# Optimization experiments

Hardware: AMD Instinct MI355X
Metric: run time of the kernel (lower is better)

The kernel has to match this reference:

```python
import jax, jax.numpy as jnp
import numpy as np

D, T, HID, Q = 33, 49, 64, 64


def _lin(x, w, b):
    return x @ w.T + b


def setup_inputs() -> dict:
    key = jax.random.key(0)
    ks = jax.random.split(key, 40)

    def nrm(k, shape, scale=0.1):
        return jax.random.normal(k, shape, jnp.float32) * scale

    vals = nrm(ks[0], (D, T), 1.0)
    mask = (jax.random.uniform(ks[1], (D, T)) < 0.8).astype(jnp.float32)
    delta = jax.random.uniform(ks[2], (D, T)) * 2.0
    data = jnp.stack([vals, mask, delta])  # [3, 33, 49]

    return {
        "data": data,
        "h0": nrm(ks[3], (HID,), 1.0),
        "H0": nrm(ks[4], (D, HID), 1.0),
        "gh_w": nrm(ks[5], (HID, D)), "gh_b": nrm(ks[6], (HID,)),
        "gst_w": nrm(ks[7], (HID, D)), "gst_b": nrm(ks[8], (HID,)),
        "gru_wih": nrm(ks[9], (3 * HID, D)), "gru_whh": nrm(ks[10], (3 * HID, HID)),
        "gru_bih": nrm(ks[11], (3 * HID,)), "gru_bhh": nrm(ks[12], (3 * HID,)),
        "wu0_w": nrm(ks[13], (Q, HID)), "wu0_b": nrm(ks[14], (Q,)),
        "wu1_w": nrm(ks[15], (Q, 2 * HID)), "wu1_b": nrm(ks[16], (Q,)),
        "wu_w": nrm(ks[17], (Q, 3 * HID)), "wu_b": nrm(ks[18], (Q,)),
        "wh_w": nrm(ks[19], (D, HID + Q)), "wh_b": nrm(ks[20], (D,)),
        "xst_w": nrm(ks[21], (1, HID)), "xst_b": nrm(ks[22], (1,)),
        "wrg_w": nrm(ks[23], (D, HID)),
        "wrs": nrm(ks[24], (1, HID)),
        "tWz": nrm(ks[25], (D, HID, HID)), "tUzx": nrm(ks[26], (D, HID, 1)), "tUzh": nrm(ks[27], (D, HID, HID)),
        "tWr": nrm(ks[28], (D, HID, HID)), "tUrx": nrm(ks[29], (D, HID, 1)), "tUrh": nrm(ks[30], (D, HID, HID)),
        "tWh": nrm(ks[31], (D, HID, HID)), "tUhx": nrm(ks[32], (D, HID, 1)), "tUhh": nrm(ks[33], (D, HID, HID)),
        "tbz": nrm(ks[34], (HID, 1)), "tbr": nrm(ks[35], (HID, 1)), "tbh": nrm(ks[36], (HID, 1)),
    }


def reference(data, h0, H0, gh_w, gh_b, gst_w, gst_b, gru_wih, gru_whh,
              gru_bih, gru_bhh, wu0_w, wu0_b, wu1_w, wu1_b, wu_w, wu_b,
              wh_w, wh_b, xst_w, xst_b, wrg_w, wrs, tWz, tUzx, tUzh,
              tWr, tUrx, tUrh, tWh, tUhx, tUhh, tbz, tbr, tbh):
    X, M, Dt = data[0], data[1], data[2]  # each (33, 49)
    h = h0          # (HID,) -> becomes (1, HID) after first GRUCell step
    H = H0          # (D, HID)
    outs, Hs, xps = [], [], []
    for t in range(T):
        x, m, d = X[:, t], M[:, t], Dt[:, t]
        # GRU-D style decay gate: exp(-max(0, Linear(delta)))
        gamma_h = jnp.exp(-jax.nn.relu(_lin(d, gh_w, gh_b)))
        h = gamma_h * h
        x_st = _lin(H, xst_w, xst_b).reshape(-1)       # (D,)
        x_st_c = m * x + (1 - m) * x_st                # imputed input
        # torch nn.GRUCell
        xi = x_st_c.reshape(1, D)
        hi = h.reshape(1, HID)
        gi = _lin(xi, gru_wih, gru_bih)
        gh_ = _lin(hi, gru_whh, gru_bhh)
        i_r, i_z, i_n = jnp.split(gi, 3, axis=1)
        h_r, h_z, h_n = jnp.split(gh_, 3, axis=1)
        r = jax.nn.sigmoid(i_r + h_r)
        z = jax.nn.sigmoid(i_z + h_z)
        n = jnp.tanh(i_n + r * h_n)
        h = (1 - z) * n + z * hi                       # (1, HID)
        # original detaches the history used for u_t
        outs.append(jax.lax.stop_gradient(h))
        if t == 0:
            u_t = _lin(h0.reshape(1, -1), wu0_w, wu0_b)
        elif t == 1:
            hd = jnp.concatenate([h0.reshape(1, -1), outs[0]], 0).reshape(1, -1)
            u_t = _lin(hd, wu1_w, wu1_b)
        elif t == 2:
            hd = jnp.concatenate([h0.reshape(1, -1), outs[0], outs[1]], 0).reshape(1, -1)
            u_t = _lin(hd, wu_w, wu_b)
        else:
            hd = jnp.concatenate(outs[t - 3:t], 0).reshape(1, -1)
            u_t = _lin(hd, wu_w, wu_b)
        x_gt_hat = _lin(jnp.concatenate([h, u_t], axis=1), wh_w, wh_b)  # (1, D)
        gamma_st = jnp.exp(-jax.nn.relu(_lin(d, gst_w, gst_b)))
        H = gamma_st * H
        # tMGRU cell: per-variable (D=33) batched matmuls
        Hr = H[:, :, None]              # (D, HID, 1)
        xr = x_st_c[:, None, None]      # (D, 1, 1)
        hr = h.reshape(HID, 1)          # (HID, 1)
        z_t = jax.nn.sigmoid(tWz @ Hr + tUzx @ xr + tUzh @ hr + tbz)
        r_t = jax.nn.sigmoid(tWr @ Hr + tUrx @ xr + tUrh @ hr + tbr)
        Hh = jnp.tanh(r_t * (tWh @ Hr) + tUhx @ xr + tUhh @ hr + tbh)
        H = (z_t * Hr + (1 - z_t) * Hh).reshape(D, HID)
        Hs.append(H)
        a = h @ wrg_w.T                 # (1, D)
        b = wrs @ H.T                   # (1, D)
        alpha1 = jax.nn.softmax(a / (a + b), axis=-1)
        alpha2 = jax.nn.softmax(b / (a + b), axis=-1)
        xps.append(alpha1 * x_gt_hat + alpha2 * x_st)  # (1, D)
    H_s = jnp.stack(Hs)                         # (T, D, HID)
    x_pred = jnp.concatenate(xps, axis=0).T     # (D, T)
    return H_s, x_pred
```

## Files before the change

### kernel.cpp

```cpp
#include <hip/hip_runtime.h>
#include <math.h>

#define DD 33
#define TT 49
#define HH 64
#define NB 33
#define NT 256

#define O_WIHT  0
#define O_WHHT  6336
#define O_GH    18624
#define O_GS    21760
#define O_WT0   24896
#define O_WT1   27008
#define O_WTG   31232
#define O_CU    37568
#define O_R     37700
#define O_PF    40936
#define PF_STRIDE 160
#define PREP_N  37700

#define SC_AGENT __HIP_MEMORY_SCOPE_AGENT

__device__ __forceinline__ float sigm(float x) {
  return 1.f / (1.f + __expf(-x));
}
__device__ __forceinline__ float ftanh(float x) {
  x = fminf(fmaxf(x, -15.f), 15.f);
  float e = __expf(2.f * x);
  return (e - 1.f) / (e + 1.f);
}

__device__ __forceinline__ float rsum64(float v) {
#pragma unroll
  for (int o = 32; o > 0; o >>= 1) v += __shfl_xor(v, o, 64);
  return v;
}
__device__ __forceinline__ float rmax64(float v) {
#pragma unroll
  for (int o = 32; o > 0; o >>= 1) v = fmaxf(v, __shfl_xor(v, o, 64));
  return v;
}

extern "C" __global__ void gmgru_prep(
    const float* __restrict__ data, const float* __restrict__ gh_w,
    const float* __restrict__ gh_b, const float* __restrict__ gst_w,
    const float* __restrict__ gst_b, const float* __restrict__ wih,
    const float* __restrict__ whh, const float* __restrict__ wu0,
    const float* __restrict__ wu0b, const float* __restrict__ wu1,
    const float* __restrict__ wu1b, const float* __restrict__ wu,
    const float* __restrict__ wub, const float* __restrict__ wh_w,
    float* __restrict__ ws) {
  int idx = blockIdx.x * blockDim.x + threadIdx.x;
  if (idx < 6336) {
    int k = idx / 192, j = idx % 192;
    ws[O_WIHT + idx] = wih[j * DD + k];
  } else if (idx < 18624) {
    int r = idx - 6336, k = r / 192, j = r % 192;
    ws[O_WHHT + r] = whh[j * HH + k];
  } else if (idx < 21760) {
    int r = idx - 18624, t = r / 64, i = r % 64;
    float s = gh_b[i];
    for (int d2 = 0; d2 < DD; ++d2)
      s += data[2 * DD * TT + d2 * TT + t] * gh_w[i * DD + d2];
    ws[O_GH + r] = expf(-fmaxf(s, 0.f));
  } else if (idx < 24896) {
    int r = idx - 21760, t = r / 64, i = r % 64;
    float s = gst_b[i];
    for (int d2 = 0; d2 < DD; ++d2)
      s += data[2 * DD * TT + d2 * TT + t] * gst_w[i * DD + d2];
    ws[O_GS + r] = expf(-fmaxf(s, 0.f));
  } else if (idx < 27008) {
    int r = idx - 24896, dd = r / 64, k = r % 64;
    float s = 0.f;
    for (int q = 0; q < 64; ++q) s += wu0[q * 64 + k] * wh_w[dd * 128 + 64 + q];
    ws[O_WT0 + r] = s;
  } else if (idx < 31232) {
    int r = idx - 27008, dd = r / 128, k = r % 128;
    float s = 0.f;
    for (int q = 0; q < 64; ++q) s += wu1[q * 128 + k] * wh_w[dd * 128 + 64 + q];
    ws[O_WT1 + r] = s;
  } else if (idx < 37568) {
    int r = idx - 31232, dd = r / 192, k = r % 192;
    float s = 0.f;
    for (int q = 0; q < 64; ++q) s += wu[q * 192 + k] * wh_w[dd * 128 + 64 + q];
    ws[O_WTG + r] = s;
  } else if (idx < PREP_N) {
    int r = idx - 37568, dd = r / 4, v = r % 4;
    float s = 0.f;
    if (v < 3) {
      const float* bp = (v == 0) ? wu0b : (v == 1) ? wu1b : wub;
      for (int q = 0; q < 64; ++q) s += bp[q] * wh_w[dd * 128 + 64 + q];
    }
    ws[O_CU + r] = s;
  }
}

extern "C" __global__ void __launch_bounds__(NT, 1)
gmgru_main(const float* __restrict__ data, const float* __restrict__ h0,
           const float* __restrict__ H0, const float* __restrict__ bih,
           const float* __restrict__ bhh, const float* __restrict__ wh_w,
           const float* __restrict__ wh_b, const float* __restrict__ xst_w,
           const float* __restrict__ xst_b, const float* __restrict__ wrg_w,
           const float* __restrict__ wrs, const float* __restrict__ tWz,
           const float* __restrict__ tUzx, const float* __restrict__ tUzh,
           const float* __restrict__ tWr, const float* __restrict__ tUrx,
           const float* __restrict__ tUrh, const float* __restrict__ tWh,
           const float* __restrict__ tUhx, const float* __restrict__ tUhh,
           const float* __restrict__ tbz, const float* __restrict__ tbr,
           const float* __restrict__ tbh, float* __restrict__ ws,
           unsigned long long* __restrict__ pf, float* __restrict__ out) {
  __shared__ float whhT_l[12288];
  __shared__ float wihT_l[6336];
  __shared__ float part[2][6][4][HH];
  __shared__ float ghL[3 * HH], giL[3 * HH];
  __shared__ float xrow[TT], mrow[TT];

  const int tid = threadIdx.x;
  const int dd = blockIdx.x;
  const int wid = tid >> 6;
  const int lane = tid & 63;

  for (int i = tid; i < 12288; i += NT) whhT_l[i] = ws[O_WHHT + i];
  for (int i = tid; i < 6336; i += NT) wihT_l[i] = ws[O_WIHT + i];
  if (tid < TT) {
    xrow[tid] = data[dd * TT + tid];
    mrow[tid] = data[DD * TT + dd * TT + tid];
  }
  float4 u0[4], u1[4], u2[4];
  {
    const int base = dd * 4096 + lane * 64 + wid * 16;
#pragma unroll
    for (int g = 0; g < 4; ++g) {
      u0[g] = *reinterpret_cast<const float4*>(tUzh + base + g * 4);
      u1[g] = *reinterpret_cast<const float4*>(tUrh + base + g * 4);
      u2[g] = *reinterpret_cast<const float4*>(tUhh + base + g * 4);
    }
  }
  const float bih_r = (tid < 192) ? bih[tid] : 0.f;
  const float bhh_r = (tid < 192) ? bhh[tid] : 0.f;
  const float ux0 = tUzx[dd * HH + lane];
  const float ux1 = tUrx[dd * HH + lane];
  const float ux2 = tUhx[dd * HH + lane];
  const float tb0 = tbz[lane];
  const float tb1 = tbr[lane];
  const float tb2 = tbh[lane];
  const float xstw_r = xst_w[lane];
  const float wrg_r = wrg_w[dd * HH + lane];
  const float wrs_r = wrs[lane];
  const float whr0_r = wh_w[dd * 128 + lane];
  const float wtg0_r = ws[O_WTG + dd * 192 + lane];
  const float wtg1_r = ws[O_WTG + dd * 192 + 64 + lane];
  const float wtg2_r = ws[O_WTG + dd * 192 + 128 + lane];
  const float wt0_r = ws[O_WT0 + dd * 64 + lane];
  const float wt1a_r = ws[O_WT1 + dd * 128 + lane];
  const float wt1b_r = ws[O_WT1 + dd * 128 + 64 + lane];
  const float cu0_r = ws[O_CU + dd * 4 + 0];
  const float cu1_r = ws[O_CU + dd * 4 + 1];
  const float cu2_r = ws[O_CU + dd * 4 + 2];
  const float whb_r = wh_b[dd];
  const float xstb_r = xst_b[0];
  const float h0s_r = h0[lane];
  float hprev = h0s_r;
  float Hrow = H0[dd * HH + lane];
  float gH_cur = ws[O_GH + lane];
  float gS_cur = ws[O_GS + lane];
  __syncthreads();

  float xst_cur = rsum64(Hrow * xstw_r) + xstb_r;
  if (wid == 0 && lane == 0) {
    float xc0 = mrow[0] * xrow[0] + (1.f - mrow[0]) * xst_cur;
    unsigned long long pk0 =
        (1ULL << 32) | (unsigned long long)__float_as_uint(xc0);
    __hip_atomic_store(&pf[(size_t)dd * PF_STRIDE], pk0, __ATOMIC_RELAXED,
                       SC_AGENT);
  }
  float xg_m1 = 0.f, xg_m2 = 0.f, xs_m1 = 0.f, xs_m2 = 0.f;
  float h1 = 0.f, h2 = 0.f, h3 = 0.f;

  for (int t = 0; t < TT; ++t) {
    const int b = t & 1;
    float hpre_r = gH_cur * hprev;
    float Hdec_r = gS_cur * Hrow;
    float gH_nxt = 0.f, gS_nxt = 0.f;
    if (t + 1 < TT) {
      gH_nxt = ws[O_GH + (t + 1) * HH + lane];
      gS_nxt = ws[O_GS + (t + 1) * HH + lane];
    }

    {
      float pw0 = 0.f, pw1 = 0.f, pw2 = 0.f;
      const int base = dd * 4096 + lane * 64 + wid * 16;
#pragma unroll
      for (int g = 0; g < 4; ++g) {
        float4 a = *reinterpret_cast<const float4*>(tWz + base + g * 4);
        float4 bb = *reinterpret_cast<const float4*>(tWr + base + g * 4);
        float4 c = *reinterpret_cast<const float4*>(tWh + base + g * 4);
        float v0 = __shfl(Hdec_r, wid * 16 + g * 4 + 0, 64);
        float v1 = __shfl(Hdec_r, wid * 16 + g * 4 + 1, 64);
        float v2 = __shfl(Hdec_r, wid * 16 + g * 4 + 2, 64);
        float v3 = __shfl(Hdec_r, wid * 16 + g * 4 + 3, 64);
        pw0 += a.x * v0 + a.y * v1 + a.z * v2 + a.w * v3;
        pw1 += bb.x * v0 + bb.y * v1 + bb.z * v2 + bb.w * v3;
        pw2 += c.x * v0 + c.y * v1 + c.z * v2 + c.w * v3;
      }
      part[b][0][wid][lane] = pw0;
      part[b][1][wid][lane] = pw1;
      part[b][2][wid][lane] = pw2;
    }
    if (tid < 3 * HH) {
      float a0 = 0.f, a1 = 0.f, a2 = 0.f, a3 = 0.f;
#pragma unroll
      for (int k = 0; k < HH; k += 4) {
        a0 += whhT_l[(k + 0) * 192 + tid] * __shfl(hpre_r, k + 0, 64);
        a1 += whhT_l[(k + 1) * 192 + tid] * __shfl(hpre_r, k + 1, 64);
        a2 += whhT_l[(k + 2) * 192 + tid] * __shfl(hpre_r, k + 2, 64);
        a3 += whhT_l[(k + 3) * 192 + tid] * __shfl(hpre_r, k + 3, 64);
      }
      ghL[tid] = bhh_r + ((a0 + a1) + (a2 + a3));
    }
    __syncthreads();

    const unsigned tagv = (unsigned)(t + 1);
    unsigned long long pk;
    for (;;) {
      pk = (lane < NB)
               ? __hip_atomic_load(&pf[(size_t)lane * PF_STRIDE + t],
                                   __ATOMIC_RELAXED, SC_AGENT)
               : (((unsigned long long)tagv) << 32);
      if (__all((int)((unsigned)(pk >> 32) == tagv))) break;
      __builtin_amdgcn_s_sleep(1);
    }
    float xcv = __uint_as_float((unsigned)(pk & 0xFFFFFFFFull));
    asm volatile("" ::: "memory");

    if (tid < 3 * HH) {
      float gi = bih_r;
#pragma unroll
      for (int k = 0; k < DD; ++k)
        gi += wihT_l[k * 192 + tid] * __shfl(xcv, k, 64);
      giL[tid] = gi;
    }
    __syncthreads();

    float rg = sigm(giL[lane] + ghL[lane]);
    float zg = sigm(giL[64 + lane] + ghL[64 + lane]);
    float ng = ftanh(giL[128 + lane] + rg * ghL[128 + lane]);
    float hn = (1.f - zg) * ng + zg * hpre_r;

    {
      float pu0 = 0.f, pu1 = 0.f, pu2 = 0.f;
#pragma unroll
      for (int g = 0; g < 4; ++g) {
        float v0 = __shfl(hn, wid * 16 + g * 4 + 0, 64);
        float v1 = __shfl(hn, wid * 16 + g * 4 + 1, 64);
        float v2 = __shfl(hn, wid * 16 + g * 4 + 2, 64);
        float v3 = __shfl(hn, wid * 16 + g * 4 + 3, 64);
        pu0 += u0[g].x * v0 + u0[g].y * v1 + u0[g].z * v2 + u0[g].w * v3;
        pu1 += u1[g].x * v0 + u1[g].y * v1 + u1[g].z * v2 + u1[g].w * v3;
        pu2 += u2[g].x * v0 + u2[g].y * v1 + u2[g].z * v2 + u2[g].w * v3;
      }
      part[b][3][wid][lane] = pu0;
      part[b][4][wid][lane] = pu1;
      part[b][5][wid][lane] = pu2;
    }
    __syncthreads();

    float r1v = -INFINITY, r2v = -INFINITY;
    if (wid == 1 && t >= 2 && lane < DD) {
      r1v = __hip_atomic_load(&ws[O_R + (t - 2) * 66 + lane], __ATOMIC_RELAXED,
                              SC_AGENT);
      r2v = __hip_atomic_load(&ws[O_R + (t - 2) * 66 + 33 + lane],
                              __ATOMIC_RELAXED, SC_AGENT);
    }

    float sz = part[b][0][0][lane] + part[b][0][1][lane] + part[b][0][2][lane] +
               part[b][0][3][lane] + part[b][3][0][lane] + part[b][3][1][lane] +
               part[b][3][2][lane] + part[b][3][3][lane];
    float sr = part[b][1][0][lane] + part[b][1][1][lane] + part[b][1][2][lane] +
               part[b][1][3][lane] + part[b][4][0][lane] + part[b][4][1][lane] +
               part[b][4][2][lane] + part[b][4][3][lane];
    float swh = part[b][2][0][lane] + part[b][2][1][lane] +
                part[b][2][2][lane] + part[b][2][3][lane];
    float suh = part[b][5][0][lane] + part[b][5][1][lane] +
                part[b][5][2][lane] + part[b][5][3][lane];
    float xc = __shfl(xcv, dd, 64);
    float z2 = sigm(sz + ux0 * xc + tb0);
    float r2g = sigm(sr + ux1 * xc + tb1);
    float hh = ftanh(r2g * swh + ux2 * xc + suh + tb2);
    float Hn = z2 * Hdec_r + (1.f - z2) * hh;

    if (wid == 0) {
      float xsn = rsum64(xstw_r * Hn);
      if (lane == 0 && t < TT - 1) {
        float xstv = xsn + xstb_r;
        float xcn = mrow[t + 1] * xrow[t + 1] + (1.f - mrow[t + 1]) * xstv;
        unsigned long long pkn =
            (((unsigned long long)(unsigned)(t + 2)) << 32) |
            (unsigned long long)__float_as_uint(xcn);
        __hip_atomic_store(&pf[(size_t)dd * PF_STRIDE + (t + 1)], pkn,
                           __ATOMIC_RELAXED, SC_AGENT);
      }
    } else if (wid == 1) {
      if (t >= 2) {
        float m1 = rmax64(r1v), m2 = rmax64(r2v);
        float e1 = (lane < DD) ? __expf(r1v - m1) : 0.f;
        float e2 = (lane < DD) ? __expf(r2v - m2) : 0.f;
        float s1 = rsum64(e1), s2 = rsum64(e2);
        float r1o = __shfl(r1v, dd, 64);
        float r2o = __shfl(r2v, dd, 64);
        if (lane == 0) {
          float a1 = __expf(r1o - m1) / s1;
          float a2 = __expf(r2o - m2) / s2;
          out[TT * DD * HH + dd * TT + (t - 2)] = a1 * xg_m2 + a2 * xs_m2;
        }
      }
      float xg = whr0_r * hn;
      if (t == 0) {
        xg += wt0_r * h0s_r;
      } else if (t == 1) {
        xg += wt1a_r * h0s_r + wt1b_r * h1;
      } else if (t == 2) {
        xg += wtg0_r * h0s_r + wtg1_r * h2 + wtg2_r * h1;
      } else {
        xg += wtg0_r * h3 + wtg1_r * h2 + wtg2_r * h1;
      }
      float xgt = rsum64(xg);
      float cu = (t == 0) ? cu0_r : (t == 1) ? cu1_r : cu2_r;
      float xsn1 = rsum64(xstw_r * Hn);
      xg_m2 = xg_m1;
      xs_m2 = xs_m1;
      xg_m1 = xgt + whb_r + cu;
      xs_m1 = xst_cur;
      xst_cur = xsn1 + xstb_r;
      h3 = h2;
      h2 = h1;
      h1 = hn;
    } else if (wid == 2) {
      float av = rsum64(wrg_r * hn);
      float bvv = rsum64(wrs_r * Hn);
      if (lane == 0) {
        float s = av + bvv;
        __hip_atomic_store(&ws[O_R + t * 66 + dd], av / s, __ATOMIC_RELAXED,
                           SC_AGENT);
        __hip_atomic_store(&ws[O_R + t * 66 + 33 + dd], bvv / s,
                           __ATOMIC_RELAXED, SC_AGENT);
      }
      asm volatile("s_waitcnt vmcnt(0)" ::: "memory");
    } else {
      out[t * DD * HH + dd * HH + lane] = Hn;
    }
    hprev = hn;
    Hrow = Hn;
    gH_cur = gH_nxt;
    gS_cur = gS_nxt;
  }

  __syncthreads();
  if (wid == 0 && lane == 0) {
    __hip_atomic_store(&pf[(size_t)dd * PF_STRIDE + TT],
                       (((unsigned long long)(unsigned)(TT + 1)) << 32),
                       __ATOMIC_RELAXED, SC_AGENT);
  }
  if (wid == 1) {
    const unsigned tagv = (unsigned)(TT + 1);
    for (;;) {
      unsigned long long pk =
          (lane < NB) ? __hip_atomic_load(&pf[(size_t)lane * PF_STRIDE + TT],
                                          __ATOMIC_RELAXED, SC_AGENT)
                      : (((unsigned long long)tagv) << 32);
      if (__all((int)((unsigned)(pk >> 32) == tagv))) break;
      __builtin_amdgcn_s_sleep(1);
    }
    asm volatile("" ::: "memory");
#pragma unroll 1
    for (int e = 0; e < 2; ++e) {
      const int step = TT - 2 + e;
      float r1v = -INFINITY, r2v = -INFINITY;
      if (lane < DD) {
        r1v = __hip_atomic_load(&ws[O_R + step * 66 + lane], __ATOMIC_RELAXED,
                                SC_AGENT);
        r2v = __hip_atomic_load(&ws[O_R + step * 66 + 33 + lane],
                                __ATOMIC_RELAXED, SC_AGENT);
      }
      float m1 = rmax64(r1v), m2 = rmax64(r2v);
      float e1 = (lane < DD) ? __expf(r1v - m1) : 0.f;
      float e2 = (lane < DD) ? __expf(r2v - m2) : 0.f;
      float s1 = rsum64(e1), s2 = rsum64(e2);
      float r1o = __shfl(r1v, dd, 64);
      float r2o = __shfl(r2v, dd, 64);
      if (lane == 0) {
        float a1 = __expf(r1o - m1) / s1;
        float a2 = __expf(r2o - m2) / s2;
        float xgv = (e == 0) ? xg_m2 : xg_m1;
        float xsv = (e == 0) ? xs_m2 : xs_m1;
        out[TT * DD * HH + dd * TT + step] = a1 * xgv + a2 * xsv;
      }
    }
  }
}

extern "C" void kernel_launch(void* const* d_in, const int* in_sizes, int n_in,
                              void* d_out, int out_size, void* d_ws,
                              size_t ws_size, hipStream_t stream) {
  (void)in_sizes; (void)n_in; (void)out_size; (void)ws_size;
  const float* data   = (const float*)d_in[0];
  const float* h0     = (const float*)d_in[1];
  const float* H0     = (const float*)d_in[2];
  const float* gh_w   = (const float*)d_in[3];
  const float* gh_b   = (const float*)d_in[4];
  const float* gst_w  = (const float*)d_in[5];
  const float* gst_b  = (const float*)d_in[6];
  const float* wih    = (const float*)d_in[7];
  const float* whh    = (const float*)d_in[8];
  const float* bih    = (const float*)d_in[9];
  const float* bhh    = (const float*)d_in[10];
  const float* wu0w   = (const float*)d_in[11];
  const float* wu0b   = (const float*)d_in[12];
  const float* wu1w   = (const float*)d_in[13];
  const float* wu1b   = (const float*)d_in[14];
  const float* wuw    = (const float*)d_in[15];
  const float* wub    = (const float*)d_in[16];
  const float* wh_w   = (const float*)d_in[17];
  const float* wh_b   = (const float*)d_in[18];
  const float* xst_w  = (const float*)d_in[19];
  const float* xst_b  = (const float*)d_in[20];
  const float* wrg_w  = (const float*)d_in[21];
  const float* wrs    = (const float*)d_in[22];
  const float* tWz    = (const float*)d_in[23];
  const float* tUzx   = (const float*)d_in[24];
  const float* tUzh   = (const float*)d_in[25];
  const float* tWr    = (const float*)d_in[26];
  const float* tUrx   = (const float*)d_in[27];
  const float* tUrh   = (const float*)d_in[28];
  const float* tWh    = (const float*)d_in[29];
  const float* tUhx   = (const float*)d_in[30];
  const float* tUhh   = (const float*)d_in[31];
  const float* tbz    = (const float*)d_in[32];
  const float* tbr    = (const float*)d_in[33];
  const float* tbh    = (const float*)d_in[34];

  float* ws = (float*)d_ws;
  unsigned long long* pf = (unsigned long long*)(ws + O_PF);

  hipMemsetAsync(pf, 0, (size_t)NB * PF_STRIDE * 8, stream);
  gmgru_prep<<<(PREP_N + 255) / 256, 256, 0, stream>>>(
      data, gh_w, gh_b, gst_w, gst_b, wih, whh, wu0w, wu0b, wu1w, wu1b, wuw,
      wub, wh_w, ws);
  gmgru_main<<<NB, NT, 0, stream>>>(
      data, h0, H0, bih, bhh, wh_w, wh_b, xst_w, xst_b, wrg_w, wrs, tWz, tUzx,
      tUzh, tWr, tUrx, tUrh, tWh, tUhx, tUhh, tbz, tbr, tbh, ws, pf,
      (float*)d_out);
}
```

Baseline: 196.3 us.

## Precompute observed-input GRU contributions and sparsify per-step input matvec over masked variables

A prep kernel now computes, for each timestep, the GRU input projection bias plus the contributions of observed (mask=1) inputs, along with a list of masked variable indices. The main loop then only adds contributions from masked variables, whose values depend on the cross-block recurrence. The GRU update runs in a single wave, with an unrolled multi-load polling loop, and is shared through LDS. This removes most of the 33x192 per-step input matvec from the serial critical path, at the cost of extra prep work, data-dependent loop lengths, and reliance on mask values being exactly 0 or 1.

```diff
diff --git a/kernel.cpp b/kernel.cpp
--- a/kernel.cpp
+++ b/kernel.cpp
@@ -16,9 +16,12 @@
 #define O_WTG   31232
 #define O_CU    37568
 #define O_R     37700
-#define O_PF    40936
+#define O_GIS   40936
+#define O_ZIDX  50344
+#define O_ZCNT  52108
+#define O_PF    52160
 #define PF_STRIDE 160
-#define PREP_N  37700
+#define PREP_N  47157
 
 #define SC_AGENT __HIP_MEMORY_SCOPE_AGENT
 
@@ -46,11 +49,11 @@
     const float* __restrict__ data, const float* __restrict__ gh_w,
     const float* __restrict__ gh_b, const float* __restrict__ gst_w,
     const float* __restrict__ gst_b, const float* __restrict__ wih,
-    const float* __restrict__ whh, const float* __restrict__ wu0,
-    const float* __restrict__ wu0b, const float* __restrict__ wu1,
-    const float* __restrict__ wu1b, const float* __restrict__ wu,
-    const float* __restrict__ wub, const float* __restrict__ wh_w,
-    float* __restrict__ ws) {
+    const float* __restrict__ bih, const float* __restrict__ whh,
+    const float* __restrict__ wu0, const float* __restrict__ wu0b,
+    const float* __restrict__ wu1, const float* __restrict__ wu1b,
+    const float* __restrict__ wu, const float* __restrict__ wub,
+    const float* __restrict__ wh_w, float* __restrict__ ws) {
   int idx = blockIdx.x * blockDim.x + threadIdx.x;
   if (idx < 6336) {
     int k = idx / 192, j = idx % 192;
@@ -85,7 +88,7 @@
     float s = 0.f;
     for (int q = 0; q < 64; ++q) s += wu[q * 192 + k] * wh_w[dd * 128 + 64 + q];
     ws[O_WTG + r] = s;
-  } else if (idx < PREP_N) {
+  } else if (idx < 37700) {
     int r = idx - 37568, dd = r / 4, v = r % 4;
     float s = 0.f;
     if (v < 3) {
@@ -93,28 +96,51 @@
       for (int q = 0; q < 64; ++q) s += bp[q] * wh_w[dd * 128 + 64 + q];
     }
     ws[O_CU + r] = s;
+  } else if (idx < 47108) {
+    int r = idx - 37700, t = r / 192, j = r % 192;
+    float s = bih[j];
+    for (int k = 0; k < DD; ++k) {
+      float mv = data[DD * TT + k * TT + t];
+      if (mv > 0.5f) s += wih[j * DD + k] * data[k * TT + t];
+    }
+    ws[O_GIS + r] = s;
+  } else if (idx < PREP_N) {
+    int t = idx - 47108;
+    int c = 0;
+    for (int k = 0; k < DD; ++k) {
+      float mv = data[DD * TT + k * TT + t];
+      if (mv < 0.5f) {
+        ws[O_ZIDX + t * 36 + c] = (float)k;
+        ++c;
+      }
+    }
+    ws[O_ZCNT + t] = (float)c;
   }
 }
 
 extern "C" __global__ void __launch_bounds__(NT, 1)
 gmgru_main(const float* __restrict__ data, const float* __restrict__ h0,
-           const float* __restrict__ H0, const float* __restrict__ bih,
-           const float* __restrict__ bhh, const float* __restrict__ wh_w,
-           const float* __restrict__ wh_b, const float* __restrict__ xst_w,
-           const float* __restrict__ xst_b, const float* __restrict__ wrg_w,
-           const float* __restrict__ wrs, const float* __restrict__ tWz,
-           const float* __restrict__ tUzx, const float* __restrict__ tUzh,
-           const float* __restrict__ tWr, const float* __restrict__ tUrx,
-           const float* __restrict__ tUrh, const float* __restrict__ tWh,
-           const float* __restrict__ tUhx, const float* __restrict__ tUhh,
-           const float* __restrict__ tbz, const float* __restrict__ tbr,
-           const float* __restrict__ tbh, float* __restrict__ ws,
-           unsigned long long* __restrict__ pf, float* __restrict__ out) {
+           const float* __restrict__ H0, const float* __restrict__ bhh,
+           const float* __restrict__ wh_w, const float* __restrict__ wh_b,
+           const float* __restrict__ xst_w, const float* __restrict__ xst_b,
+           const float* __restrict__ wrg_w, const float* __restrict__ wrs,
+           const float* __restrict__ tWz, const float* __restrict__ tUzx,
+           const float* __restrict__ tUzh, const float* __restrict__ tWr,
+           const float* __restrict__ tUrx, const float* __restrict__ tUrh,
+           const float* __restrict__ tWh, const float* __restrict__ tUhx,
+           const float* __restrict__ tUhh, const float* __restrict__ tbz,
+           const float* __restrict__ tbr, const float* __restrict__ tbh,
+           float* __restrict__ ws, unsigned long long* __restrict__ pf,
+           float* __restrict__ out) {
   __shared__ float whhT_l[12288];
   __shared__ float wihT_l[6336];
   __shared__ float part[2][6][4][HH];
-  __shared__ float ghL[3 * HH], giL[3 * HH];
+  __shared__ float ghL[3 * HH];
+  __shared__ float hnewL[HH];
   __shared__ float xrow[TT], mrow[TT];
+  __shared__ float xcdd[2];
+  __shared__ signed char zidxL[TT * 36];
+  __shared__ signed char zcntL[TT];
 
   const int tid = threadIdx.x;
   const int dd = blockIdx.x;
@@ -126,6 +152,10 @@
   if (tid < TT) {
     xrow[tid] = data[dd * TT + tid];
     mrow[tid] = data[DD * TT + dd * TT + tid];
+    int c = (int)ws[O_ZCNT + tid];
+    zcntL[tid] = (signed char)c;
+    for (int j = 0; j < c; ++j)
+      zidxL[tid * 36 + j] = (signed char)(int)ws[O_ZIDX + tid * 36 + j];
   }
   float4 u0[4], u1[4], u2[4];
   {
@@ -137,7 +167,6 @@
       u2[g] = *reinterpret_cast<const float4*>(tUhh + base + g * 4);
     }
   }
-  const float bih_r = (tid < 192) ? bih[tid] : 0.f;
   const float bhh_r = (tid < 192) ? bhh[tid] : 0.f;
   const float ux0 = tUzx[dd * HH + lane];
   const float ux1 = tUrx[dd * HH + lane];
@@ -170,6 +199,7 @@
   float xst_cur = rsum64(Hrow * xstw_r) + xstb_r;
   if (wid == 0 && lane == 0) {
     float xc0 = mrow[0] * xrow[0] + (1.f - mrow[0]) * xst_cur;
+    xcdd[0] = xc0;
     unsigned long long pk0 =
         (1ULL << 32) | (unsigned long long)__float_as_uint(xc0);
     __hip_atomic_store(&pf[(size_t)dd * PF_STRIDE], pk0, __ATOMIC_RELAXED,
@@ -182,10 +212,19 @@
     const int b = t & 1;
     float hpre_r = gH_cur * hprev;
     float Hdec_r = gS_cur * Hrow;
-    float gH_nxt = 0.f, gS_nxt = 0.f;
+    float gH_nxt = 0.f, gS_nxt = 0.f, xmn = 0.f, omn = 0.f;
     if (t + 1 < TT) {
       gH_nxt = ws[O_GH + (t + 1) * HH + lane];
       gS_nxt = ws[O_GS + (t + 1) * HH + lane];
+      float mv = mrow[t + 1];
+      xmn = mv * xrow[t + 1];
+      omn = 1.f - mv;
+    }
+    float gis0 = 0.f, gis1 = 0.f, gis2 = 0.f;
+    if (wid == 0) {
+      gis0 = ws[O_GIS + t * 192 + lane];
+      gis1 = ws[O_GIS + t * 192 + 64 + lane];
+      gis2 = ws[O_GIS + t * 192 + 128 + lane];
     }
 
     {
@@ -221,41 +260,59 @@
     }
     __syncthreads();
 
-    const unsigned tagv = (unsigned)(t + 1);
-    unsigned long long pk;
-    for (;;) {
-      pk = (lane < NB)
-               ? __hip_atomic_load(&pf[(size_t)lane * PF_STRIDE + t],
-                                   __ATOMIC_RELAXED, SC_AGENT)
-               : (((unsigned long long)tagv) << 32);
-      if (__all((int)((unsigned)(pk >> 32) == tagv))) break;
-      __builtin_amdgcn_s_sleep(1);
-    }
-    float xcv = __uint_as_float((unsigned)(pk & 0xFFFFFFFFull));
-    asm volatile("" ::: "memory");
-
-    if (tid < 3 * HH) {
-      float gi = bih_r;
-#pragma unroll
-      for (int k = 0; k < DD; ++k)
-        gi += wihT_l[k * 192 + tid] * __shfl(xcv, k, 64);
-      giL[tid] = gi;
+    if (wid == 0) {
+      const unsigned tagv = (unsigned)(t + 1);
+      const unsigned long long fab = ((unsigned long long)tagv) << 32;
+      auto pollLd = [&]() -> unsigned long long {
+        return (lane < NB)
+                   ? __hip_atomic_load(&pf[(size_t)lane * PF_STRIDE + t],
+                                       __ATOMIC_RELAXED, SC_AGENT)
+                   : fab;
+      };
+      unsigned long long pk;
+      {
+        unsigned long long q0 = pollLd(), q1 = pollLd(), q2 = pollLd(),
+                           q3 = pollLd();
+        for (;;) {
+          if (__all((int)((unsigned)(q0 >> 32) == tagv))) { pk = q0; break; }
+          q0 = pollLd();
+          if (__all((int)((unsigned)(q1 >> 32) == tagv))) { pk = q1; break; }
+          q1 = pollLd();
+          if (__all((int)((unsigned)(q2 >> 32) == tagv))) { pk = q2; break; }
+          q2 = pollLd();
+          if (__all((int)((unsigned)(q3 >> 32) == tagv))) { pk = q3; break; }
+          q3 = pollLd();
+        }
+      }
+      float xcv = __uint_as_float((unsigned)(pk & 0xFFFFFFFFull));
+      asm volatile("" ::: "memory");
+      float gr = gis0, gz = gis1, gn = gis2;
+      const int zc = (int)zcntL[t];
+#pragma unroll 1
+      for (int j = 0; j < zc; ++j) {
+        const int k = (int)zidxL[t * 36 + j];
+        float xk = __shfl(xcv, k, 64);
+        gr += wihT_l[k * 192 + lane] * xk;
+        gz += wihT_l[k * 192 + 64 + lane] * xk;
+        gn += wihT_l[k * 192 + 128 + lane] * xk;
+      }
+      float rg = sigm(gr + ghL[lane]);
+      float zg = sigm(gz + ghL[64 + lane]);
+      float ng = ftanh(gn + rg * ghL[128 + lane]);
+      hnewL[lane] = (1.f - zg) * ng + zg * hpre_r;
     }
     __syncthreads();
 
-    float rg = sigm(giL[lane] + ghL[lane]);
-    float zg = sigm(giL[64 + lane] + ghL[64 + lane]);
-    float ng = ftanh(giL[128 + lane] + rg * ghL[128 + lane]);
-    float hn = (1.f - zg) * ng + zg * hpre_r;
+    const float hn = hnewL[lane];
 
     {
       float pu0 = 0.f, pu1 = 0.f, pu2 = 0.f;
 #pragma unroll
       for (int g = 0; g < 4; ++g) {
-        float v0 = __shfl(hn, wid * 16 + g * 4 + 0, 64);
-        float v1 = __shfl(hn, wid * 16 + g * 4 + 1, 64);
-        float v2 = __shfl(hn, wid * 16 + g * 4 + 2, 64);
-        float v3 = __shfl(hn, wid * 16 + g * 4 + 3, 64);
+        float v0 = hnewL[wid * 16 + g * 4 + 0];
+        float v1 = hnewL[wid * 16 + g * 4 + 1];
+        float v2 = hnewL[wid * 16 + g * 4 + 2];
+        float v3 = hnewL[wid * 16 + g * 4 + 3];
         pu0 += u0[g].x * v0 + u0[g].y * v1 + u0[g].z * v2 + u0[g].w * v3;
         pu1 += u1[g].x * v0 + u1[g].y * v1 + u1[g].z * v2 + u1[g].w * v3;
         pu2 += u2[g].x * v0 + u2[g].y * v1 + u2[g].z * v2 + u2[g].w * v3;
@@ -284,7 +341,7 @@
                 part[b][2][2][lane] + part[b][2][3][lane];
     float suh = part[b][5][0][lane] + part[b][5][1][lane] +
                 part[b][5][2][lane] + part[b][5][3][lane];
-    float xc = __shfl(xcv, dd, 64);
+    float xc = xcdd[b];
     float z2 = sigm(sz + ux0 * xc + tb0);
     float r2g = sigm(sr + ux1 * xc + tb1);
     float hh = ftanh(r2g * swh + ux2 * xc + suh + tb2);
@@ -294,7 +351,8 @@
       float xsn = rsum64(xstw_r * Hn);
       if (lane == 0 && t < TT - 1) {
         float xstv = xsn + xstb_r;
-        float xcn = mrow[t + 1] * xrow[t + 1] + (1.f - mrow[t + 1]) * xstv;
+        float xcn = xmn + omn * xstv;
+        xcdd[(t + 1) & 1] = xcn;
         unsigned long long pkn =
             (((unsigned long long)(unsigned)(t + 2)) << 32) |
             (unsigned long long)__float_as_uint(xcn);
@@ -445,10 +503,10 @@
 
   hipMemsetAsync(pf, 0, (size_t)NB * PF_STRIDE * 8, stream);
   gmgru_prep<<<(PREP_N + 255) / 256, 256, 0, stream>>>(
-      data, gh_w, gh_b, gst_w, gst_b, wih, whh, wu0w, wu0b, wu1w, wu1b, wuw,
-      wub, wh_w, ws);
+      data, gh_w, gh_b, gst_w, gst_b, wih, bih, whh, wu0w, wu0b, wu1w, wu1b,
+      wuw, wub, wh_w, ws);
   gmgru_main<<<NB, NT, 0, stream>>>(
-      data, h0, H0, bih, bhh, wh_w, wh_b, xst_w, xst_b, wrg_w, wrs, tWz, tUzx,
+      data, h0, H0, bhh, wh_w, wh_b, xst_w, xst_b, wrg_w, wrs, tWz, tUzx,
       tUzh, tWr, tUrx, tUrh, tWh, tUhx, tUhh, tbz, tbr, tbh, ws, pf,
       (float*)d_out);
 }
```

Result: slower. 221.9 us (+13.1%).
